# Performance work log

Hardware: AMD Instinct MI355X
Metric: run time of the kernel (lower is better)

## Reference

```python
import jax, jax.numpy as jnp
import numpy as np

BS, LS, NWRD, D, H, NTGT, MC = 32, 512, 100000, 128, 512, 2048, 20
TEMP = 0.5  # gumbel-softmax temperature (self.last_t)
HLOSS_COEF = 0.03


def setup_inputs() -> dict:
    key = jax.random.key(0)
    ks = jax.random.split(key, 12)
    inp_word = jax.random.randint(ks[0], (BS, LS), 0, NWRD, dtype=jnp.int32)
    inp_char = jax.random.randint(ks[1], (BS, LS, MC), 0, 95, dtype=jnp.int32)
    inp_pos = jax.random.randint(ks[2], (BS, LS), 0, 50, dtype=jnp.int32)
    keyword_table = jax.random.bernoulli(ks[3], 0.1, (NWRD,))  # wid in keywords_set
    tgt_ids = jax.random.randint(ks[4], (NTGT,), 0, NWRD, dtype=jnp.int32)
    lut = jax.random.randint(ks[5], (NWRD, MC), 0, 95, dtype=jnp.int32)
    u = jax.random.uniform(ks[6], (BS, LS, NTGT), minval=1e-6, maxval=1.0 - 1e-6)
    gumbel = -jnp.log(-jnp.log(u))  # standard Gumbel(0,1) noise
    W = jax.random.normal(ks[7], (NWRD, D), dtype=jnp.float32) * 0.02
    W1 = jax.random.normal(ks[8], (D, H), dtype=jnp.float32) * (1.0 / np.sqrt(D))
    b1 = jnp.zeros((H,), jnp.float32)
    W2 = jax.random.normal(ks[9], (H, NTGT), dtype=jnp.float32) * (1.0 / np.sqrt(H))
    b2 = jnp.zeros((NTGT,), jnp.float32)
    return dict(inp_word=inp_word, inp_char=inp_char, inp_pos=inp_pos,
                keyword_table=keyword_table, tgt_ids=tgt_ids, lut=lut,
                gumbel=gumbel, W=W, W1=W1, b1=b1, W2=W2, b2=b2)


def reference(inp_word, inp_char, inp_pos, keyword_table, tgt_ids, lut,
              gumbel, W, W1, b1, W2, b2):
    # keyword membership mask (idx in the original; torch gathers only masked
    # spots -- here we compute densely and select with the mask, same math at
    # every masked position, identity elsewhere)
    mask = keyword_table[inp_word]                      # [bs, ls] bool

    x = W[inp_word]                                     # embed: [bs, ls, d]
    hdn = jax.nn.relu(jnp.einsum('bsd,dh->bsh', x, W1) + b1)
    logits = jnp.einsum('bsh,ht->bst', hdn, W2) + b2    # [bs, ls, ntgt]

    # log_p.masked_scatter_(idx, x.max(-1)[0])
    log_p = jnp.where(mask, logits.max(axis=-1), 0.0)

    # hloss: mean entropy over masked spots * 0.03
    lsm = jax.nn.log_softmax(logits, axis=-1)
    ent = -jnp.sum(jnp.exp(lsm) * lsm, axis=-1)         # [bs, ls]
    n_spots = jnp.maximum(mask.sum(), 1)
    loss_h = (ent * mask).sum() / n_spots * HLOSS_COEF

    # gumbel_softmax(x, t): softmax((logits + g) / t)
    sft = jax.nn.softmax((logits + gumbel) / TEMP, axis=-1)  # [bs, ls, ntgt]

    # hard pick mapped through tgtwords, scattered into word
    y = tgt_ids[jnp.argmax(sft, axis=-1)]               # [bs, ls]
    word = jnp.where(mask, y, inp_word)

    # soft embedding: sft @ word_emb_tgt, word_emb_tgt = W[tgt_ids]
    x_emb = jnp.einsum('bst,td->bsd', sft, W[tgt_ids])  # [bs, ls, d]
    word_emb = jnp.where(mask[..., None], x_emb, x)     # scatter into W[word]

    char = lut[word]                                    # word_to_char lookup

    return (mask.astype(jnp.float32), log_p, word, char, word_emb, loss_h)
```

## Files before the change

kernel.cpp:

```cpp
#include <hip/hip_runtime.h>
#include <cstdint>

#define R_TOT 16384
#define T_NT  2048
#define DD    128
#define HH    512
#define MC_   20
#define BR    16
#define NBLK  1024
#define SPW   16

#define MASK_OFF 0
#define LOGP_OFF 16384
#define WORD_OFF 32768
#define CHAR_OFF 49152
#define EMB_OFF  376832
#define LOSS_OFF 2473984

#define HDN_OFF   0
#define HDNB_OFF  8388608
#define W2T_OFF   12582912
#define W2Q_OFF   13631488
#define WTT5_OFF  14155776
#define WT_OFF    14286848
#define ENT_OFF   14548992
#define CNT_OFF   14550016
#define S_OFF     14551040
#define WS_NEED_FLOATS (S_OFF + 16777216)

typedef __attribute__((ext_vector_type(8))) short short8v;
typedef __attribute__((ext_vector_type(4))) float f32x4;
typedef unsigned short ushort_t;

__device__ __forceinline__ ushort_t f2bf(float f) {
    union { float f; unsigned int u; } v; v.f = f;
    unsigned int r = v.u + 0x7FFFu + ((v.u >> 16) & 1u);
    return (ushort_t)(r >> 16);
}
__device__ __forceinline__ float bf2f(ushort_t u) {
    union { unsigned int u; float f; } v; v.u = ((unsigned int)u) << 16;
    return v.f;
}
__device__ __forceinline__ void stage16(const ushort_t* gsrc, ushort_t* ldst) {
    __builtin_amdgcn_global_load_lds(
        (const __attribute__((address_space(1))) unsigned int*)gsrc,
        (__attribute__((address_space(3))) unsigned int*)ldst, 16, 0, 0);
}

__global__ __launch_bounds__(256) void k1_gather(
    const int* __restrict__ tgt_ids, const float* __restrict__ W, float* __restrict__ wtgt)
{
    int rr = blockIdx.x * 2 + (threadIdx.x >> 7);
    int d = threadIdx.x & 127;
    int wsrc = tgt_ids[rr];
    wtgt[(size_t)rr * DD + d] = W[(size_t)wsrc * DD + d];
}

__global__ __launch_bounds__(256) void k1b_wtgtT5(
    const float* __restrict__ wtgt, ushort_t* __restrict__ wtgtT5)
{
    const int sc = blockIdx.x, t = threadIdx.x;
    #pragma unroll
    for (int it = 0; it < 2; ++it) {
        int idx = it * 256 + t;
        int df = idx >> 6, lane = idx & 63;
        int lrow = lane & 15, kg = lane >> 4;
        ushort_t* dst = wtgtT5 + ((size_t)sc * 8 + df) * 512 + lane * 8;
        #pragma unroll
        for (int j = 0; j < 8; ++j) {
            int col = sc * 32 + (j < 4 ? kg * 4 + j : 16 + kg * 4 + (j - 4));
            dst[j] = f2bf(wtgt[(size_t)col * DD + df * 16 + lrow]);
        }
    }
}

__global__ __launch_bounds__(256) void k0_w2t(
    const float* __restrict__ W2, float* __restrict__ W2Tf, ushort_t* __restrict__ W2q)
{
    __shared__ float tile[32][33];
    const int js = blockIdx.x, ks = blockIdx.y;
    const int cb = js * 32, kb = ks * 32;
    const int lx = threadIdx.x & 31, ly = threadIdx.x >> 5;
    #pragma unroll
    for (int i = 0; i < 32; i += 8)
        tile[ly + i][lx] = W2[(size_t)(kb + ly + i) * T_NT + cb + lx];
    __syncthreads();
    #pragma unroll
    for (int i = 0; i < 32; i += 8) {
        int c = cb + ly + i, k = kb + lx;
        W2Tf[(size_t)c * HH + k] = tile[lx][ly + i];
    }
    if (threadIdx.x < 128) {
        int c = threadIdx.x >> 2, kgrp = threadIdx.x & 3;
        int cs = c >> 4, lrow = c & 15;
        ushort_t* dst = W2q + (size_t)(((js * 2 + cs) * 16 + ks) * 512) + (kgrp * 16 + lrow) * 8;
        #pragma unroll
        for (int i = 0; i < 8; ++i)
            dst[i] = f2bf(tile[kgrp * 8 + i][c]);
    }
}

__global__ __launch_bounds__(256) void k2_hdn(
    const int* __restrict__ inp_word, const float* __restrict__ W,
    const float* __restrict__ W1, const float* __restrict__ b1,
    float* __restrict__ hdn, ushort_t* __restrict__ hdnB)
{
    __shared__ float As[16][64];
    __shared__ float Bs[16][64];
    const int t = threadIdx.x;
    const int bm = blockIdx.x * 64;
    const int bn = blockIdx.y * 64;
    const int tx = t & 15, ty = t >> 4;
    float acc[4][4] = {};
    for (int k0 = 0; k0 < DD; k0 += 16) {
        {
            int m = t >> 2, kq = t & 3;
            int wsrc = inp_word[bm + m];
            float4 v = *(const float4*)(W + (size_t)wsrc * DD + k0 + kq * 4);
            As[kq * 4 + 0][m] = v.x; As[kq * 4 + 1][m] = v.y;
            As[kq * 4 + 2][m] = v.z; As[kq * 4 + 3][m] = v.w;
        }
        {
            int k = t >> 4, nq = t & 15;
            *(float4*)(&Bs[k][nq * 4]) =
                *(const float4*)(W1 + (size_t)(k0 + k) * HH + bn + nq * 4);
        }
        __syncthreads();
        #pragma unroll
        for (int k = 0; k < 16; ++k) {
            float a[4], b[4];
            #pragma unroll
            for (int i = 0; i < 4; i++) a[i] = As[k][ty * 4 + i];
            #pragma unroll
            for (int j = 0; j < 4; j++) b[j] = Bs[k][tx * 4 + j];
            #pragma unroll
            for (int i = 0; i < 4; i++)
                #pragma unroll
                for (int j = 0; j < 4; j++)
                    acc[i][j] = fmaf(a[i], b[j], acc[i][j]);
        }
        __syncthreads();
    }
    #pragma unroll
    for (int i = 0; i < 4; i++) {
        int m = bm + ty * 4 + i;
        int n = bn + tx * 4;
        float4 v;
        v.x = fmaxf(acc[i][0] + b1[n + 0], 0.f);
        v.y = fmaxf(acc[i][1] + b1[n + 1], 0.f);
        v.z = fmaxf(acc[i][2] + b1[n + 2], 0.f);
        v.w = fmaxf(acc[i][3] + b1[n + 3], 0.f);
        *(float4*)(hdn + (size_t)m * HH + n) = v;
        ushort4 hb;
        hb.x = f2bf(v.x); hb.y = f2bf(v.y); hb.z = f2bf(v.z); hb.w = f2bf(v.w);
        *(ushort4*)(hdnB + (size_t)m * HH + n) = hb;
    }
}

__global__ __launch_bounds__(256) void k3a_gemm(
    const ushort_t* __restrict__ hdnB, const ushort_t* __restrict__ W2q,
    ushort_t* __restrict__ S)
{
    __shared__ ushort_t aT[2 * 4096];
    __shared__ ushort_t bT[2 * 4096];

    const int t = threadIdx.x;
    const int wid = t >> 6, lane = t & 63;
    const int lrow = lane & 15, kgrp = lane >> 4;
    const int nb = blockIdx.x, mb = blockIdx.y;
    const int wr = wid >> 1, wc = wid & 1;

    f32x4 acc[4][4];
    #pragma unroll
    for (int r = 0; r < 4; ++r)
        #pragma unroll
        for (int c = 0; c < 4; ++c) acc[r][c] = (f32x4){0.f, 0.f, 0.f, 0.f};

    #define K3A_STAGE(buf, ks)                                                          \
        {                                                                               \
            _Pragma("unroll")                                                           \
            for (int i = 0; i < 2; ++i) {                                               \
                int g = wid * 2 + i;                                                    \
                const ushort_t* asrc = hdnB + (size_t)(mb * 128 + g * 16 + lrow) * HH   \
                                       + (ks) * 32 + kgrp * 8;                          \
                stage16(asrc, &aT[(buf) * 4096 + g * 512 + lane * 8]);                  \
                const ushort_t* bsrc = W2q + (size_t)(((nb * 8 + g) * 16 + (ks)) * 512) \
                                       + lane * 8;                                      \
                stage16(bsrc, &bT[(buf) * 4096 + g * 512 + lane * 8]);                  \
            }                                                                           \
        }

    K3A_STAGE(0, 0);
    __syncthreads();

    for (int ks = 0; ks < 16; ++ks) {
        const int buf = ks & 1;
        if (ks + 1 < 16) K3A_STAGE(buf ^ 1, ks + 1);

        short8v af[4], bf[4];
        #pragma unroll
        for (int r = 0; r < 4; ++r)
            af[r] = *(const short8v*)&aT[buf * 4096 + (wr * 4 + r) * 512 + lane * 8];
        #pragma unroll
        for (int c = 0; c < 4; ++c)
            bf[c] = *(const short8v*)&bT[buf * 4096 + (wc * 4 + c) * 512 + lane * 8];

        #pragma unroll
        for (int r = 0; r < 4; ++r)
            #pragma unroll
            for (int c = 0; c < 4; ++c)
                acc[r][c] = __builtin_amdgcn_mfma_f32_16x16x32_bf16(bf[c], af[r], acc[r][c], 0, 0, 0);

        __syncthreads();
    }

    #pragma unroll
    for (int r = 0; r < 4; ++r) {
        #pragma unroll
        for (int c = 0; c < 4; ++c) {
            int row = mb * 128 + wr * 64 + r * 16 + lrow;
            int col = nb * 128 + wc * 64 + c * 16 + kgrp * 4;
            ushort4 o;
            o.x = f2bf(acc[r][c][0]); o.y = f2bf(acc[r][c][1]);
            o.z = f2bf(acc[r][c][2]); o.w = f2bf(acc[r][c][3]);
            *(ushort4*)(S + (size_t)row * T_NT + col) = o;
        }
    }
    #undef K3A_STAGE
}

__global__ __launch_bounds__(256) void k3bc(
    const ushort_t* __restrict__ S, const float* __restrict__ hdn,
    const float* __restrict__ W2Tf, const float* __restrict__ b2,
    const float* __restrict__ gumbel, const int* __restrict__ inp_word,
    const int* __restrict__ keyword_table, const int* __restrict__ tgt_ids,
    const int* __restrict__ lut, const float* __restrict__ W,
    const ushort_t* __restrict__ wtgtT5,
    float* __restrict__ out, float* __restrict__ entP, float* __restrict__ cntP)
{
    __shared__ ushort_t PS[16 * 2056];
    __shared__ float invs2S[16], entS[16];
    __shared__ int   mskS[16], winS[16], candS[32];

    const int t = threadIdx.x;
    const int wid = t >> 6, lane = t & 63;
    const int lrow = lane & 15, kgrp = lane >> 4;
    const int row0 = blockIdx.x * BR;

    for (int r = 0; r < 4; ++r) {
        const int rl = wid * 4 + r;
        const int grow = row0 + rl;
        const ushort_t* sR = S + (size_t)grow * T_NT;
        const float* gR = gumbel + (size_t)grow * T_NT;
        float m_ = -1e30f, sE_ = 0.f, sEl_ = 0.f, s2_ = 0.f;
        float a1_ = -1e30f, a2_ = -1e30f;
        int i1_ = 0, i2_ = 0;
        #pragma unroll
        for (int ch = 0; ch < 4; ++ch) {
            const int col = ch * 512 + lane * 8;
            ushort_t sv[8];
            *(uint4*)sv = *(const uint4*)(sR + col);
            float g[8];
            *(float4*)(g + 0) = *(const float4*)(gR + col);
            *(float4*)(g + 4) = *(const float4*)(gR + col + 4);
            float bb[8];
            *(float4*)(bb + 0) = *(const float4*)(b2 + col);
            *(float4*)(bb + 4) = *(const float4*)(b2 + col + 4);
            ushort_t pv[8];
            #pragma unroll
            for (int j = 0; j < 8; ++j) {
                float l = bf2f(sv[j]) + bb[j];
                m_ = fmaxf(m_, l);
                float e = __expf(l);
                sE_ += e; sEl_ = fmaf(e, l, sEl_);
                float a = l + g[j];
                float p = __expf(2.0f * a);
                s2_ += p;
                int ci = col + j;
                if (a > a1_) { a2_ = a1_; i2_ = i1_; a1_ = a; i1_ = ci; }
                else if (a > a2_) { a2_ = a; i2_ = ci; }
                pv[j] = f2bf(p);
            }
            *(uint4*)(&PS[rl * 2056 + col]) = *(uint4*)pv;
        }
        #pragma unroll
        for (int mk = 1; mk < 64; mk <<= 1) {
            m_ = fmaxf(m_, __shfl_xor(m_, mk));
            sE_ += __shfl_xor(sE_, mk);
            sEl_ += __shfl_xor(sEl_, mk);
            s2_ += __shfl_xor(s2_, mk);
            float ob1 = __shfl_xor(a1_, mk); int oj1 = __shfl_xor(i1_, mk);
            float ob2 = __shfl_xor(a2_, mk); int oj2 = __shfl_xor(i2_, mk);
            if (ob1 > a1_ || (ob1 == a1_ && oj1 < i1_)) {
                if (a1_ > ob2 || (a1_ == ob2 && i1_ < oj2)) { a2_ = a1_; i2_ = i1_; }
                else { a2_ = ob2; i2_ = oj2; }
                a1_ = ob1; i1_ = oj1;
            } else {
                if (ob1 > a2_) { a2_ = ob1; i2_ = oj1; }
            }
        }
        if (lane == 0) {
            int w_in = inp_word[grow];
            int msk = keyword_table[w_in] != 0;
            out[MASK_OFF + grow] = msk ? 1.0f : 0.0f;
            out[LOGP_OFF + grow] = msk ? m_ : 0.0f;
            invs2S[rl] = 1.0f / s2_;
            mskS[rl] = msk; winS[rl] = w_in;
            entS[rl] = msk ? (__logf(sE_) - sEl_ / sE_) : 0.0f;
            candS[rl * 2 + 0] = i1_;
            candS[rl * 2 + 1] = i2_;
        }
    }
    __syncthreads();

    {
        const int df0 = wid * 2;
        f32x4 acc0 = (f32x4){0.f, 0.f, 0.f, 0.f}, acc1 = acc0;
        const ushort_t* pBase = &PS[lrow * 2056 + kgrp * 4];
        const ushort_t* vB = wtgtT5 + (size_t)df0 * 512 + lane * 8;
        for (int sc = 0; sc < 64; ++sc) {
            ushort4 pa = *(const ushort4*)(pBase + sc * 32);
            ushort4 pb = *(const ushort4*)(pBase + sc * 32 + 16);
            short8v pav;
            pav[0] = (short)pa.x; pav[1] = (short)pa.y; pav[2] = (short)pa.z; pav[3] = (short)pa.w;
            pav[4] = (short)pb.x; pav[5] = (short)pb.y; pav[6] = (short)pb.z; pav[7] = (short)pb.w;
            const ushort_t* vt = vB + (size_t)sc * 4096;
            short8v bv0 = *(const short8v*)vt;
            short8v bv1 = *(const short8v*)(vt + 512);
            acc0 = __builtin_amdgcn_mfma_f32_16x16x32_bf16(pav, bv0, acc0, 0, 0, 0);
            acc1 = __builtin_amdgcn_mfma_f32_16x16x32_bf16(pav, bv1, acc1, 0, 0, 0);
        }
        #pragma unroll
        for (int q = 0; q < 4; ++q) {
            int rl = kgrp * 4 + q;
            int grow = row0 + rl;
            float inv = invs2S[rl];
            int msk = mskS[rl], w_in = winS[rl];
            int d0 = df0 * 16 + lrow;
            float v0 = msk ? acc0[q] * inv : W[(size_t)w_in * DD + d0];
            out[EMB_OFF + (size_t)grow * DD + d0] = v0;
            int d1 = d0 + 16;
            float v1 = msk ? acc1[q] * inv : W[(size_t)w_in * DD + d1];
            out[EMB_OFF + (size_t)grow * DD + d1] = v1;
        }
    }

    for (int rr = wid; rr < BR; rr += 4) {
        int grow = row0 + rr;
        int i1 = candS[rr * 2 + 0], i2 = candS[rr * 2 + 1];
        int mskr = mskS[rr];
        const float* hrow = hdn + (size_t)grow * HH;
        float4 h0 = *(const float4*)(hrow + lane * 8);
        float4 h1 = *(const float4*)(hrow + lane * 8 + 4);
        float v1, v2;
        {
            const float* wrow = W2Tf + (size_t)i1 * HH;
            float4 w0 = *(const float4*)(wrow + lane * 8);
            float4 w1 = *(const float4*)(wrow + lane * 8 + 4);
            float sdot = h0.x*w0.x + h0.y*w0.y + h0.z*w0.z + h0.w*w0.w
                       + h1.x*w1.x + h1.y*w1.y + h1.z*w1.z + h1.w*w1.w;
            #pragma unroll
            for (int mk = 1; mk < 64; mk <<= 1) sdot += __shfl_xor(sdot, mk);
            v1 = sdot + b2[i1] + gumbel[(size_t)grow * T_NT + i1];
        }
        {
            const float* wrow = W2Tf + (size_t)i2 * HH;
            float4 w0 = *(const float4*)(wrow + lane * 8);
            float4 w1 = *(const float4*)(wrow + lane * 8 + 4);
            float sdot = h0.x*w0.x + h0.y*w0.y + h0.z*w0.z + h0.w*w0.w
                       + h1.x*w1.x + h1.y*w1.y + h1.z*w1.z + h1.w*w1.w;
            #pragma unroll
            for (int mk = 1; mk < 64; mk <<= 1) sdot += __shfl_xor(sdot, mk);
            v2 = sdot + b2[i2] + gumbel[(size_t)grow * T_NT + i2];
        }
        int ibest = (v2 > v1 || (v2 == v1 && i2 < i1)) ? i2 : i1;
        int word = mskr ? tgt_ids[ibest] : winS[rr];
        if (lane == 0) out[WORD_OFF + grow] = (float)word;
        if (lane < MC_)
            out[CHAR_OFF + (size_t)grow * MC_ + lane] = (float)lut[(size_t)word * MC_ + lane];
    }

    if (t == 0) {
        float es = 0.f; int cs = 0;
        #pragma unroll
        for (int r = 0; r < BR; r++) { es += entS[r]; cs += mskS[r]; }
        entP[blockIdx.x] = es;
        cntP[blockIdx.x] = (float)cs;
    }
}

__global__ __launch_bounds__(256) void k3_fused_fb(
    const ushort_t* __restrict__ hdnB, const float* __restrict__ hdn,
    const ushort_t* __restrict__ W2q, const float* __restrict__ W2Tf,
    const float* __restrict__ b2, const float* __restrict__ gumbel,
    const int* __restrict__ inp_word, const int* __restrict__ keyword_table,
    const int* __restrict__ tgt_ids, const int* __restrict__ lut,
    const float* __restrict__ W, const ushort_t* __restrict__ wtgtT5,
    float* __restrict__ out, float* __restrict__ entP, float* __restrict__ cntP)
{
    __shared__ float bigS[6144];
    __shared__ float statP[4][16][8];
    __shared__ int   candS[BR * 2];
    __shared__ float invs2S[BR], entS[BR];
    __shared__ int   mskS[BR], winS[BR];

    const int t = threadIdx.x;
    const int wid = t >> 6, lane = t & 63;
    const int lrow = lane & 15, kgrp = lane >> 4;
    const int row0 = blockIdx.x * BR;

    ushort_t* aP = (ushort_t*)bigS;
    #pragma unroll
    for (int it = 0; it < 4; ++it) {
        int gid = it * 256 + t;
        int ks = gid >> 6, l2 = gid & 63;
        int lr = l2 & 15, kg = l2 >> 4;
        uint4 v = *(const uint4*)(hdnB + (size_t)(row0 + lr) * HH + ks * 32 + kg * 8);
        *(uint4*)(aP + gid * 8) = v;
    }
    __syncthreads();

    const int scq = (int)((blockIdx.x + wid) & 3);
    const ushort_t* aRd = aP + lane * 8;
    const float* gRow = gumbel + (size_t)(row0 + lrow) * T_NT + kgrp * 4;

    float m_ = -1e30f, sE_ = 0.f, sEl_ = 0.f, s2_ = 0.f;
    float a1_ = -1e30f, a2_ = -1e30f;
    int i1_ = 0, i2_ = 0;
    f32x4 accpv[8];
    #pragma unroll
    for (int df = 0; df < 8; ++df) accpv[df] = (f32x4){0.f, 0.f, 0.f, 0.f};

    f32x4 ga = *(const f32x4*)(gRow + scq * 32);
    f32x4 gb = *(const f32x4*)(gRow + scq * 32 + 16);

    for (int s = 0; s < SPW; ++s) {
        const int sc = scq + 4 * s;
        const int scn = scq + 4 * ((s + 1) & 15);
        f32x4 gna = *(const f32x4*)(gRow + scn * 32);
        f32x4 gnb = *(const f32x4*)(gRow + scn * 32 + 16);
        f32x4 b2a = *(const f32x4*)(b2 + sc * 32 + kgrp * 4);
        f32x4 b2b = *(const f32x4*)(b2 + sc * 32 + kgrp * 4 + 16);

        const ushort_t* w2a = W2q + (size_t)sc * 16384 + lane * 8;
        f32x4 c0a = (f32x4){0.f,0.f,0.f,0.f}, c0b = c0a, c1a = c0a, c1b = c0a;
        #pragma unroll
        for (int ks = 0; ks < 16; ks += 2) {
            short8v avk0 = *(const short8v*)(aRd + (ks + 0) * 512);
            short8v avk1 = *(const short8v*)(aRd + (ks + 1) * 512);
            c0a = __builtin_amdgcn_mfma_f32_16x16x32_bf16(*(const short8v*)(w2a + (ks+0)*512), avk0, c0a, 0, 0, 0);
            c1a = __builtin_amdgcn_mfma_f32_16x16x32_bf16(*(const short8v*)(w2a + 8192 + (ks+0)*512), avk0, c1a, 0, 0, 0);
            c0b = __builtin_amdgcn_mfma_f32_16x16x32_bf16(*(const short8v*)(w2a + (ks+1)*512), avk1, c0b, 0, 0, 0);
            c1b = __builtin_amdgcn_mfma_f32_16x16x32_bf16(*(const short8v*)(w2a + 8192 + (ks+1)*512), avk1, c1b, 0, 0, 0);
        }
        f32x4 acc0 = c0a + c0b;
        f32x4 acc1 = c1a + c1b;

        const ushort_t* vt = wtgtT5 + (size_t)sc * 4096 + lane * 8;
        short8v bvf[8];
        #pragma unroll
        for (int df = 0; df < 8; ++df) bvf[df] = *(const short8v*)(vt + df * 512);

        short8v pav;
        const int colb = sc * 32 + kgrp * 4;
        #pragma unroll
        for (int q = 0; q < 4; ++q) {
            float l0 = acc0[q] + b2a[q];
            m_ = fmaxf(m_, l0);
            float e0 = __expf(l0);
            sE_ += e0; sEl_ = fmaf(e0, l0, sEl_);
            float aa0 = l0 + ga[q];
            float p0 = __expf(2.0f * aa0);
            s2_ += p0;
            if (aa0 > a1_) { a2_ = a1_; i2_ = i1_; a1_ = aa0; i1_ = colb + q; }
            else if (aa0 > a2_) { a2_ = aa0; i2_ = colb + q; }
            pav[q] = (short)f2bf(p0);
            float l1 = acc1[q] + b2b[q];
            m_ = fmaxf(m_, l1);
            float e1 = __expf(l1);
            sE_ += e1; sEl_ = fmaf(e1, l1, sEl_);
            float aa1 = l1 + gb[q];
            float p1 = __expf(2.0f * aa1);
            s2_ += p1;
            if (aa1 > a1_) { a2_ = a1_; i2_ = i1_; a1_ = aa1; i1_ = colb + 16 + q; }
            else if (aa1 > a2_) { a2_ = aa1; i2_ = colb + 16 + q; }
            pav[4 + q] = (short)f2bf(p1);
        }

        #pragma unroll
        for (int df = 0; df < 8; ++df)
            accpv[df] = __builtin_amdgcn_mfma_f32_16x16x32_bf16(pav, bvf[df], accpv[df], 0, 0, 0);

        ga = gna; gb = gnb;
    }

    #pragma unroll
    for (int mk = 16; mk < 64; mk <<= 1) {
        m_ = fmaxf(m_, __shfl_xor(m_, mk));
        sE_ += __shfl_xor(sE_, mk);
        sEl_ += __shfl_xor(sEl_, mk);
        s2_ += __shfl_xor(s2_, mk);
        float ob1 = __shfl_xor(a1_, mk); int oj1 = __shfl_xor(i1_, mk);
        float ob2 = __shfl_xor(a2_, mk); int oj2 = __shfl_xor(i2_, mk);
        if (ob1 > a1_ || (ob1 == a1_ && oj1 < i1_)) {
            if (a1_ > ob2 || (a1_ == ob2 && i1_ < oj2)) { a2_ = a1_; i2_ = i1_; }
            else { a2_ = ob2; i2_ = oj2; }
            a1_ = ob1; i1_ = oj1;
        } else {
            if (ob1 > a2_) { a2_ = ob1; i2_ = oj1; }
        }
    }

    __syncthreads();
    if (lane < 16) {
        float* st = &statP[wid][lane][0];
        st[0] = m_; st[1] = sE_; st[2] = sEl_; st[3] = s2_;
        st[4] = a1_; st[5] = __int_as_float(i1_);
        st[6] = a2_; st[7] = __int_as_float(i2_);
    }
    if (wid >= 1) {
        float* scr = bigS + (wid - 1) * 2048;
        #pragma unroll
        for (int df = 0; df < 8; ++df)
            #pragma unroll
            for (int q = 0; q < 4; ++q)
                scr[(kgrp * 4 + q) * 128 + df * 16 + lrow] = accpv[df][q];
    }
    __syncthreads();

    if (wid == 0) {
        if (lane < 16) {
            float M = -1e30f, SE = 0.f, SEL = 0.f, S2 = 0.f;
            float A1 = -1e30f, A2 = -1e30f; int I1 = 0, I2 = 0;
            #pragma unroll
            for (int w = 0; w < 4; ++w) {
                const float* st = &statP[w][lane][0];
                float ob1 = st[4]; int oj1 = __float_as_int(st[5]);
                float ob2 = st[6]; int oj2 = __float_as_int(st[7]);
                M = fmaxf(M, st[0]); SE += st[1]; SEL += st[2]; S2 += st[3];
                if (ob1 > A1 || (ob1 == A1 && oj1 < I1)) {
                    if (A1 > ob2 || (A1 == ob2 && I1 < oj2)) { A2 = A1; I2 = I1; }
                    else { A2 = ob2; I2 = oj2; }
                    A1 = ob1; I1 = oj1;
                } else {
                    if (ob1 > A2) { A2 = ob1; I2 = oj1; }
                }
            }
            int grow = row0 + lane;
            int w_in = inp_word[grow];
            int msk = keyword_table[w_in] != 0;
            out[MASK_OFF + grow] = msk ? 1.0f : 0.0f;
            out[LOGP_OFF + grow] = msk ? M : 0.0f;
            invs2S[lane] = 1.0f / S2;
            mskS[lane] = msk;
            winS[lane] = w_in;
            entS[lane] = msk ? (__logf(SE) - SEL / SE) : 0.0f;
            candS[lane * 2 + 0] = I1;
            candS[lane * 2 + 1] = I2;
        }
        #pragma unroll
        for (int df = 0; df < 8; ++df)
            #pragma unroll
            for (int q = 0; q < 4; ++q)
                accpv[df][q] += bigS[0 * 2048 + (kgrp * 4 + q) * 128 + df * 16 + lrow]
                              + bigS[1 * 2048 + (kgrp * 4 + q) * 128 + df * 16 + lrow]
                              + bigS[2 * 2048 + (kgrp * 4 + q) * 128 + df * 16 + lrow];
    }
    __syncthreads();

    if (wid == 0) {
        #pragma unroll
        for (int df = 0; df < 8; ++df) {
            #pragma unroll
            for (int q = 0; q < 4; ++q) {
                int rl = kgrp * 4 + q;
                int grow = row0 + rl;
                int d = df * 16 + lrow;
                float val = accpv[df][q] * invs2S[rl];
                if (!mskS[rl]) val = W[(size_t)winS[rl] * DD + d];
                out[EMB_OFF + (size_t)grow * DD + d] = val;
            }
        }
    }

    for (int rr = wid; rr < BR; rr += 4) {
        int grow = row0 + rr;
        int i1 = candS[rr * 2 + 0], i2 = candS[rr * 2 + 1];
        int mskr = mskS[rr];
        const float* hrow = hdn + (size_t)grow * HH;
        float4 h0 = *(const float4*)(hrow + lane * 8);
        float4 h1 = *(const float4*)(hrow + lane * 8 + 4);
        float v1, v2;
        {
            const float* wrow = W2Tf + (size_t)i1 * HH;
            float4 w0 = *(const float4*)(wrow + lane * 8);
            float4 w1 = *(const float4*)(wrow + lane * 8 + 4);
            float sdot = h0.x*w0.x + h0.y*w0.y + h0.z*w0.z + h0.w*w0.w
                       + h1.x*w1.x + h1.y*w1.y + h1.z*w1.z + h1.w*w1.w;
            #pragma unroll
            for (int mk = 1; mk < 64; mk <<= 1) sdot += __shfl_xor(sdot, mk);
            v1 = sdot + b2[i1] + gumbel[(size_t)grow * T_NT + i1];
        }
        {
            const float* wrow = W2Tf + (size_t)i2 * HH;
            float4 w0 = *(const float4*)(wrow + lane * 8);
            float4 w1 = *(const float4*)(wrow + lane * 8 + 4);
            float sdot = h0.x*w0.x + h0.y*w0.y + h0.z*w0.z + h0.w*w0.w
                       + h1.x*w1.x + h1.y*w1.y + h1.z*w1.z + h1.w*w1.w;
            #pragma unroll
            for (int mk = 1; mk < 64; mk <<= 1) sdot += __shfl_xor(sdot, mk);
            v2 = sdot + b2[i2] + gumbel[(size_t)grow * T_NT + i2];
        }
        int ibest = (v2 > v1 || (v2 == v1 && i2 < i1)) ? i2 : i1;
        int word = mskr ? tgt_ids[ibest] : winS[rr];
        if (lane == 0) out[WORD_OFF + grow] = (float)word;
        if (lane < MC_)
            out[CHAR_OFF + (size_t)grow * MC_ + lane] = (float)lut[(size_t)word * MC_ + lane];
    }

    if (t == 0) {
        float es = 0.f; int cs = 0;
        #pragma unroll
        for (int r = 0; r < BR; r++) { es += entS[r]; cs += mskS[r]; }
        entP[blockIdx.x] = es;
        cntP[blockIdx.x] = (float)cs;
    }
}

__global__ __launch_bounds__(256) void k4_loss(
    const float* __restrict__ entP, const float* __restrict__ cntP, float* __restrict__ out)
{
    __shared__ float sE[256], sC[256];
    int t = threadIdx.x;
    float e = 0.f, c = 0.f;
    for (int i = t; i < NBLK; i += 256) { e += entP[i]; c += cntP[i]; }
    sE[t] = e; sC[t] = c;
    __syncthreads();
    for (int s = 128; s > 0; s >>= 1) {
        if (t < s) { sE[t] += sE[t + s]; sC[t] += sC[t + s]; }
        __syncthreads();
    }
    if (t == 0) {
        float ns = fmaxf(sC[0], 1.0f);
        out[LOSS_OFF] = 0.03f * sE[0] / ns;
    }
}

extern "C" void kernel_launch(void* const* d_in, const int* in_sizes, int n_in,
                              void* d_out, int out_size, void* d_ws, size_t ws_size,
                              hipStream_t stream) {
    const int* inp_word = (const int*)d_in[0];
    const int* keyword_table = (const int*)d_in[3];
    const int* tgt_ids = (const int*)d_in[4];
    const int* lut = (const int*)d_in[5];
    const float* gumbel = (const float*)d_in[6];
    const float* W = (const float*)d_in[7];
    const float* W1 = (const float*)d_in[8];
    const float* b1 = (const float*)d_in[9];
    const float* W2 = (const float*)d_in[10];
    const float* b2 = (const float*)d_in[11];
    float* out = (float*)d_out;

    float* wsf = (float*)d_ws;
    float* hdn = wsf + HDN_OFF;
    ushort_t* hdnB = (ushort_t*)(wsf + HDNB_OFF);
    float* W2Tf = wsf + W2T_OFF;
    ushort_t* W2q = (ushort_t*)(wsf + W2Q_OFF);
    ushort_t* wtgtT5 = (ushort_t*)(wsf + WTT5_OFF);
    float* wtgt = wsf + WT_OFF;
    float* entP = wsf + ENT_OFF;
    float* cntP = wsf + CNT_OFF;
    ushort_t* S = (ushort_t*)(wsf + S_OFF);

    k1_gather<<<T_NT / 2, 256, 0, stream>>>(tgt_ids, W, wtgt);
    k1b_wtgtT5<<<64, 256, 0, stream>>>(wtgt, wtgtT5);
    k0_w2t<<<dim3(T_NT / 32, HH / 32), 256, 0, stream>>>(W2, W2Tf, W2q);
    k2_hdn<<<dim3(R_TOT / 64, HH / 64), 256, 0, stream>>>(inp_word, W, W1, b1, hdn, hdnB);

    if (ws_size >= (size_t)WS_NEED_FLOATS * sizeof(float)) {
        k3a_gemm<<<dim3(16, 128), 256, 0, stream>>>(hdnB, W2q, S);
        k3bc<<<NBLK, 256, 0, stream>>>(S, hdn, W2Tf, b2, gumbel,
                                       inp_word, keyword_table, tgt_ids, lut,
                                       W, wtgtT5, out, entP, cntP);
    } else {
        k3_fused_fb<<<NBLK, 256, 0, stream>>>(hdnB, hdn, W2q, W2Tf, b2, gumbel,
                                              inp_word, keyword_table, tgt_ids, lut,
                                              W, wtgtT5, out, entP, cntP);
    }
    k4_loss<<<1, 256, 0, stream>>>(entP, cntP, out);
}
```

Baseline: 196.1 us.

## Interleave softmax-probability staging with MFMA soft-embedding in column chunks

Restructures k3bc so that softmax probabilities are computed and staged in LDS one 512-column chunk at a time. The MFMA soft-embedding accumulation for each chunk runs right after it, instead of staging all 2048 columns and then doing one long MFMA loop. This cuts the LDS buffer from about 64KB to about 16KB, which should allow more resident blocks per CU and interleave load/exp work with matrix work. In exchange it adds two block barriers per chunk and keeps per-row reduction state in registers for four rows at once, which raises register pressure.

```diff
diff --git a/kernel.cpp b/kernel.cpp
--- a/kernel.cpp
+++ b/kernel.cpp
@@ -238,7 +238,7 @@
     const ushort_t* __restrict__ wtgtT5,
     float* __restrict__ out, float* __restrict__ entP, float* __restrict__ cntP)
 {
-    __shared__ ushort_t PS[16 * 2056];
+    __shared__ ushort_t PS[16 * 520];
     __shared__ float invs2S[16], entS[16];
     __shared__ int   mskS[16], winS[16], candS[32];
 
@@ -247,22 +247,29 @@
     const int lrow = lane & 15, kgrp = lane >> 4;
     const int row0 = blockIdx.x * BR;
 
+    float m_[4], sE_[4], sEl_[4], s2_[4], a1_[4], a2_[4];
+    int i1_[4], i2_[4];
+    #pragma unroll
     for (int r = 0; r < 4; ++r) {
-        const int rl = wid * 4 + r;
-        const int grow = row0 + rl;
-        const ushort_t* sR = S + (size_t)grow * T_NT;
-        const float* gR = gumbel + (size_t)grow * T_NT;
-        float m_ = -1e30f, sE_ = 0.f, sEl_ = 0.f, s2_ = 0.f;
-        float a1_ = -1e30f, a2_ = -1e30f;
-        int i1_ = 0, i2_ = 0;
-        #pragma unroll
-        for (int ch = 0; ch < 4; ++ch) {
-            const int col = ch * 512 + lane * 8;
+        m_[r] = -1e30f; sE_[r] = 0.f; sEl_[r] = 0.f; s2_[r] = 0.f;
+        a1_[r] = -1e30f; a2_[r] = -1e30f; i1_[r] = 0; i2_[r] = 0;
+    }
+    f32x4 acc0 = (f32x4){0.f, 0.f, 0.f, 0.f}, acc1 = acc0;
+    const int df0 = wid * 2;
+    const ushort_t* vB = wtgtT5 + (size_t)df0 * 512 + lane * 8;
+    const ushort_t* pBase = &PS[lrow * 520 + kgrp * 4];
+
+    for (int ch = 0; ch < 4; ++ch) {
+        const int col = ch * 512 + lane * 8;
+        #pragma unroll
+        for (int r = 0; r < 4; ++r) {
+            const int rl = wid * 4 + r;
+            const int grow = row0 + rl;
             ushort_t sv[8];
-            *(uint4*)sv = *(const uint4*)(sR + col);
+            *(uint4*)sv = *(const uint4*)(S + (size_t)grow * T_NT + col);
             float g[8];
-            *(float4*)(g + 0) = *(const float4*)(gR + col);
-            *(float4*)(g + 4) = *(const float4*)(gR + col + 4);
+            *(float4*)(g + 0) = *(const float4*)(gumbel + (size_t)grow * T_NT + col);
+            *(float4*)(g + 4) = *(const float4*)(gumbel + (size_t)grow * T_NT + col + 4);
             float bb[8];
             *(float4*)(bb + 0) = *(const float4*)(b2 + col);
             *(float4*)(bb + 4) = *(const float4*)(b2 + col + 4);
@@ -270,79 +277,83 @@
             #pragma unroll
             for (int j = 0; j < 8; ++j) {
                 float l = bf2f(sv[j]) + bb[j];
-                m_ = fmaxf(m_, l);
+                m_[r] = fmaxf(m_[r], l);
                 float e = __expf(l);
-                sE_ += e; sEl_ = fmaf(e, l, sEl_);
+                sE_[r] += e; sEl_[r] = fmaf(e, l, sEl_[r]);
                 float a = l + g[j];
                 float p = __expf(2.0f * a);
-                s2_ += p;
+                s2_[r] += p;
                 int ci = col + j;
-                if (a > a1_) { a2_ = a1_; i2_ = i1_; a1_ = a; i1_ = ci; }
-                else if (a > a2_) { a2_ = a; i2_ = ci; }
+                if (a > a1_[r]) { a2_[r] = a1_[r]; i2_[r] = i1_[r]; a1_[r] = a; i1_[r] = ci; }
+                else if (a > a2_[r]) { a2_[r] = a; i2_[r] = ci; }
                 pv[j] = f2bf(p);
             }
-            *(uint4*)(&PS[rl * 2056 + col]) = *(uint4*)pv;
-        }
+            *(uint4*)(&PS[rl * 520 + lane * 8]) = *(uint4*)pv;
+        }
+        __syncthreads();
+
+        const ushort_t* vt = vB + (size_t)(ch * 16) * 4096;
+        #pragma unroll
+        for (int sci = 0; sci < 16; ++sci) {
+            ushort4 pa = *(const ushort4*)(pBase + sci * 32);
+            ushort4 pb = *(const ushort4*)(pBase + sci * 32 + 16);
+            short8v pav;
+            pav[0] = (short)pa.x; pav[1] = (short)pa.y; pav[2] = (short)pa.z; pav[3] = (short)pa.w;
+            pav[4] = (short)pb.x; pav[5] = (short)pb.y; pav[6] = (short)pb.z; pav[7] = (short)pb.w;
+            short8v bv0 = *(const short8v*)(vt + sci * 4096);
+            short8v bv1 = *(const short8v*)(vt + sci * 4096 + 512);
+            acc0 = __builtin_amdgcn_mfma_f32_16x16x32_bf16(pav, bv0, acc0, 0, 0, 0);
+            acc1 = __builtin_amdgcn_mfma_f32_16x16x32_bf16(pav, bv1, acc1, 0, 0, 0);
+        }
+        __syncthreads();
+    }
+
+    #pragma unroll
+    for (int r = 0; r < 4; ++r) {
         #pragma unroll
         for (int mk = 1; mk < 64; mk <<= 1) {
-            m_ = fmaxf(m_, __shfl_xor(m_, mk));
-            sE_ += __shfl_xor(sE_, mk);
-            sEl_ += __shfl_xor(sEl_, mk);
-            s2_ += __shfl_xor(s2_, mk);
-            float ob1 = __shfl_xor(a1_, mk); int oj1 = __shfl_xor(i1_, mk);
-            float ob2 = __shfl_xor(a2_, mk); int oj2 = __shfl_xor(i2_, mk);
-            if (ob1 > a1_ || (ob1 == a1_ && oj1 < i1_)) {
-                if (a1_ > ob2 || (a1_ == ob2 && i1_ < oj2)) { a2_ = a1_; i2_ = i1_; }
-                else { a2_ = ob2; i2_ = oj2; }
-                a1_ = ob1; i1_ = oj1;
+            m_[r] = fmaxf(m_[r], __shfl_xor(m_[r], mk));
+            sE_[r] += __shfl_xor(sE_[r], mk);
+            sEl_[r] += __shfl_xor(sEl_[r], mk);
+            s2_[r] += __shfl_xor(s2_[r], mk);
+            float ob1 = __shfl_xor(a1_[r], mk); int oj1 = __shfl_xor(i1_[r], mk);
+            float ob2 = __shfl_xor(a2_[r], mk); int oj2 = __shfl_xor(i2_[r], mk);
+            if (ob1 > a1_[r] || (ob1 == a1_[r] && oj1 < i1_[r])) {
+                if (a1_[r] > ob2 || (a1_[r] == ob2 && i1_[r] < oj2)) { a2_[r] = a1_[r]; i2_[r] = i1_[r]; }
+                else { a2_[r] = ob2; i2_[r] = oj2; }
+                a1_[r] = ob1; i1_[r] = oj1;
             } else {
-                if (ob1 > a2_) { a2_ = ob1; i2_ = oj1; }
+                if (ob1 > a2_[r]) { a2_[r] = ob1; i2_[r] = oj1; }
             }
         }
         if (lane == 0) {
+            int rl = wid * 4 + r;
+            int grow = row0 + rl;
             int w_in = inp_word[grow];
             int msk = keyword_table[w_in] != 0;
             out[MASK_OFF + grow] = msk ? 1.0f : 0.0f;
-            out[LOGP_OFF + grow] = msk ? m_ : 0.0f;
-            invs2S[rl] = 1.0f / s2_;
+            out[LOGP_OFF + grow] = msk ? m_[r] : 0.0f;
+            invs2S[rl] = 1.0f / s2_[r];
             mskS[rl] = msk; winS[rl] = w_in;
-            entS[rl] = msk ? (__logf(sE_) - sEl_ / sE_) : 0.0f;
-            candS[rl * 2 + 0] = i1_;
-            candS[rl * 2 + 1] = i2_;
+            entS[rl] = msk ? (__logf(sE_[r]) - sEl_[r] / sE_[r]) : 0.0f;
+            candS[rl * 2 + 0] = i1_[r];
+            candS[rl * 2 + 1] = i2_[r];
         }
     }
     __syncthreads();
 
-    {
-        const int df0 = wid * 2;
-        f32x4 acc0 = (f32x4){0.f, 0.f, 0.f, 0.f}, acc1 = acc0;
-        const ushort_t* pBase = &PS[lrow * 2056 + kgrp * 4];
-        const ushort_t* vB = wtgtT5 + (size_t)df0 * 512 + lane * 8;
-        for (int sc = 0; sc < 64; ++sc) {
-            ushort4 pa = *(const ushort4*)(pBase + sc * 32);
-            ushort4 pb = *(const ushort4*)(pBase + sc * 32 + 16);
-            short8v pav;
-            pav[0] = (short)pa.x; pav[1] = (short)pa.y; pav[2] = (short)pa.z; pav[3] = (short)pa.w;
-            pav[4] = (short)pb.x; pav[5] = (short)pb.y; pav[6] = (short)pb.z; pav[7] = (short)pb.w;
-            const ushort_t* vt = vB + (size_t)sc * 4096;
-            short8v bv0 = *(const short8v*)vt;
-            short8v bv1 = *(const short8v*)(vt + 512);
-            acc0 = __builtin_amdgcn_mfma_f32_16x16x32_bf16(pav, bv0, acc0, 0, 0, 0);
-            acc1 = __builtin_amdgcn_mfma_f32_16x16x32_bf16(pav, bv1, acc1, 0, 0, 0);
-        }
-        #pragma unroll
-        for (int q = 0; q < 4; ++q) {
-            int rl = kgrp * 4 + q;
-            int grow = row0 + rl;
-            float inv = invs2S[rl];
-            int msk = mskS[rl], w_in = winS[rl];
-            int d0 = df0 * 16 + lrow;
-            float v0 = msk ? acc0[q] * inv : W[(size_t)w_in * DD + d0];
-            out[EMB_OFF + (size_t)grow * DD + d0] = v0;
-            int d1 = d0 + 16;
-            float v1 = msk ? acc1[q] * inv : W[(size_t)w_in * DD + d1];
-            out[EMB_OFF + (size_t)grow * DD + d1] = v1;
-        }
+    #pragma unroll
+    for (int q = 0; q < 4; ++q) {
+        int rl = kgrp * 4 + q;
+        int grow = row0 + rl;
+        float inv = invs2S[rl];
+        int msk = mskS[rl], w_in = winS[rl];
+        int d0 = df0 * 16 + lrow;
+        float v0 = msk ? acc0[q] * inv : W[(size_t)w_in * DD + d0];
+        out[EMB_OFF + (size_t)grow * DD + d0] = v0;
+        int d1 = d0 + 16;
+        float v1 = msk ? acc1[q] * inv : W[(size_t)w_in * DD + d1];
+        out[EMB_OFF + (size_t)grow * DD + d1] = v1;
     }
 
     for (int rr = wid; rr < BR; rr += 4) {
```

Measured after the change: 218.5 us. 11.4% more time.
